# Optimization experiments

Measured on AMD Instinct MI355X. Metric: run time of the kernel, lower is better.

## Reference

```python
import jax, jax.numpy as jnp
import numpy as np

EMBED_DIM = 1024
NUM_HEADS = 16
RANK = 32
HEAD_DIM = EMBED_DIM // NUM_HEADS
SCALE = 1.0 / np.sqrt(RANK).astype(np.float32)


def setup_inputs() -> dict:
    key = jax.random.key(0)
    ks = jax.random.split(key, 9)
    B, S = 2, 2048
    def lin(k, fan_in, fan_out):
        bound = 1.0 / np.sqrt(fan_in)
        return jax.random.uniform(k, (fan_in, fan_out), jnp.float32, -bound, bound)
    return {
        "hidden_states": jax.random.normal(ks[0], (B, S, EMBED_DIM), jnp.float32),
        "Wq": lin(ks[1], EMBED_DIM, RANK * NUM_HEADS),
        "bq": jnp.zeros((RANK * NUM_HEADS,), jnp.float32),
        "Wk": lin(ks[2], EMBED_DIM, RANK * NUM_HEADS),
        "bk": jnp.zeros((RANK * NUM_HEADS,), jnp.float32),
        "Wv": lin(ks[3], EMBED_DIM, EMBED_DIM),
        "bv": jnp.zeros((EMBED_DIM,), jnp.float32),
        "Wo": lin(ks[4], EMBED_DIM, EMBED_DIM),
        "bo": jnp.zeros((EMBED_DIM,), jnp.float32),
    }


def reference(hidden_states, Wq, bq, Wk, bk, Wv, bv, Wo, bo):
    B, S, E = hidden_states.shape
    q = (hidden_states @ Wq + bq).reshape(B, S, NUM_HEADS, RANK)      # [b,i,h,r]
    k = (hidden_states @ Wk + bk).reshape(B, S, NUM_HEADS, RANK)      # [b,j,h,r]
    v = (hidden_states @ Wv + bv).reshape(B, S, NUM_HEADS, HEAD_DIM)  # [b,j,h,d]
    # full [b,i,j,h] score tensor, softmax over j (axis=2), as in the torch code
    scores = jnp.einsum('bihr,bjhr->bijh', q, k) * SCALE
    attn = jax.nn.softmax(scores, axis=2)
    out = jnp.einsum('bijh,bjhd->bihd', attn, v).reshape(B, S, E)
    return out @ Wo + bo
```

## Files before the change

### kernel.cpp

```cpp
#include <hip/hip_runtime.h>

#define EMBED   1024
#define NHEADS  16
#define RANK    32
#define HDIM    64
#define BATCH   2
#define SEQ     2048
#define BSQ     (BATCH * SEQ)
#define CEXP    0.25505998f

typedef __attribute__((ext_vector_type(8))) short bf16x8;
typedef __attribute__((ext_vector_type(4))) float f32x4;
typedef __attribute__((ext_vector_type(8))) _Float16 f16x8;

__device__ __forceinline__ float bf2f(unsigned short u) {
    union { unsigned int i; float f; } x; x.i = ((unsigned int)u) << 16;
    return x.f;
}
__device__ __forceinline__ unsigned short f2bf(float f) {
    union { float f; unsigned int i; } x; x.f = f;
    unsigned int r = x.i + 0x7FFFu + ((x.i >> 16) & 1u);
    return (unsigned short)(r >> 16);
}

#define ASYNC16(gp, lp) \
    __builtin_amdgcn_global_load_lds( \
        (const __attribute__((address_space(1))) void*)(gp), \
        (__attribute__((address_space(3))) void*)(lp), 16, 0, 0)

__global__ __launch_bounds__(256) void prep_all(
    const float* __restrict__ hs,
    const float* __restrict__ Wq, const float* __restrict__ Wk,
    const float* __restrict__ Wv, const float* __restrict__ Wo,
    const float* __restrict__ bq, const float* __restrict__ bk,
    const float* __restrict__ bv,
    unsigned short* __restrict__ hsb, unsigned short* __restrict__ wT_all,
    unsigned short* __restrict__ woT, float* __restrict__ ball)
{
    __shared__ float L[64][65];
    const int blk = blockIdx.x;
    const int t = threadIdx.x;

    if (blk < 2048) {
        const size_t i = ((size_t)blk * 256 + t) * 8;
        float4 v0 = *(const float4*)(hs + i);
        float4 v1 = *(const float4*)(hs + i + 4);
        ushort4 o0, o1;
        o0.x = f2bf(v0.x); o0.y = f2bf(v0.y); o0.z = f2bf(v0.z); o0.w = f2bf(v0.w);
        o1.x = f2bf(v1.x); o1.y = f2bf(v1.y); o1.z = f2bf(v1.z); o1.w = f2bf(v1.w);
        *(ushort4*)(hsb + i) = o0;
        *(ushort4*)(hsb + i + 4) = o1;
        return;
    }
    if (blk < 2816) {
        int idx = blk - 2048;
        int z, bx, by;
        if (idx < 256) { z = idx >> 7; int r2 = idx & 127; bx = r2 & 7; by = r2 >> 3; }
        else { idx -= 256; z = 2 + (idx >> 8); int r2 = idx & 255; bx = r2 & 15; by = r2 >> 4; }
        const int Nw = (z < 2) ? 512 : 1024;
        const float* W = (z == 0) ? Wq : (z == 1) ? Wk : (z == 2) ? Wv : Wo;
        unsigned short* dst = (z == 3) ? woT : (wT_all + (size_t)z * 512 * 1024);

        const int r = t >> 2, c0 = (t & 3) * 16;
        const float* src = W + (size_t)(by * 64 + r) * Nw + bx * 64 + c0;
        #pragma unroll
        for (int u = 0; u < 4; u++)
            *(float4*)&L[r][c0 + 4 * u] = *(const float4*)(src + 4 * u);
        __syncthreads();
        unsigned short* drow = dst + (size_t)(bx * 64 + r) * 1024 + by * 64 + c0;
        #pragma unroll
        for (int u4 = 0; u4 < 4; u4++) {
            ushort4 o;
            o.x = f2bf(L[c0 + 4 * u4 + 0][r]);
            o.y = f2bf(L[c0 + 4 * u4 + 1][r]);
            o.z = f2bf(L[c0 + 4 * u4 + 2][r]);
            o.w = f2bf(L[c0 + 4 * u4 + 3][r]);
            *(ushort4*)(drow + 4 * u4) = o;
        }
        return;
    }
    {
        const int i = (blk - 2816) * 256 + t;
        ball[i] = (i < 512) ? bq[i] : (i < 1024) ? bk[i - 512] : bv[i - 1024];
    }
}

template <bool OUT_F32>
__global__ __launch_bounds__(256) void gemm_mfma(
    const unsigned short* __restrict__ A, const unsigned short* __restrict__ BT,
    const float* __restrict__ bias, void* __restrict__ Cv,
    unsigned short* __restrict__ qH, unsigned short* __restrict__ kH,
    unsigned short* __restrict__ vTout, int N)
{
    __shared__ unsigned short As[128 * 32];
    __shared__ unsigned short Bs[128 * 32];
    const int K = 1024;
    const int t = threadIdx.x;
    const int lane = t & 63;
    const int li = lane & 15, la = lane >> 4;
    const int w = t >> 6, wm = w >> 1, wn = w & 1;
    const int row0 = blockIdx.y * 128, col0 = blockIdx.x * 128;

    const int sr = lane >> 2, sc2 = (lane & 3) * 8;
    const unsigned short* ag0 = A + (size_t)(row0 + w * 32 + sr) * K + sc2;
    const unsigned short* ag1 = A + (size_t)(row0 + w * 32 + 16 + sr) * K + sc2;
    const unsigned short* bg0 = BT + (size_t)(col0 + w * 32 + sr) * K + sc2;
    const unsigned short* bg1 = BT + (size_t)(col0 + w * 32 + 16 + sr) * K + sc2;
    unsigned short* lA0 = &As[(w * 32) * 32];
    unsigned short* lA1 = &As[(w * 32 + 16) * 32];
    unsigned short* lB0 = &Bs[(w * 32) * 32];
    unsigned short* lB1 = &Bs[(w * 32 + 16) * 32];

    f32x4 acc[4][4];
    #pragma unroll
    for (int i = 0; i < 4; i++)
        #pragma unroll
        for (int j = 0; j < 4; j++)
            acc[i][j] = (f32x4){0.f, 0.f, 0.f, 0.f};

    for (int k0 = 0; k0 < K; k0 += 32) {
        ASYNC16(ag0 + k0, lA0);
        ASYNC16(ag1 + k0, lA1);
        ASYNC16(bg0 + k0, lB0);
        ASYNC16(bg1 + k0, lB1);
        __syncthreads();
        bf16x8 af[4], bfr[4];
        #pragma unroll
        for (int mt = 0; mt < 4; mt++)
            af[mt] = *(const bf16x8*)&As[(wm * 64 + mt * 16 + li) * 32 + la * 8];
        #pragma unroll
        for (int nt = 0; nt < 4; nt++)
            bfr[nt] = *(const bf16x8*)&Bs[(wn * 64 + nt * 16 + li) * 32 + la * 8];
        #pragma unroll
        for (int mt = 0; mt < 4; mt++)
            #pragma unroll
            for (int nt = 0; nt < 4; nt++)
                acc[mt][nt] = __builtin_amdgcn_mfma_f32_16x16x32_bf16(af[mt], bfr[nt], acc[mt][nt], 0, 0, 0);
        __syncthreads();
    }

    if (OUT_F32) {
        #pragma unroll
        for (int nt = 0; nt < 4; nt++) {
            const int col = col0 + wn * 64 + nt * 16 + li;
            const float bval = bias[col];
            #pragma unroll
            for (int mt = 0; mt < 4; mt++)
                #pragma unroll
                for (int r = 0; r < 4; r++) {
                    const int row = row0 + wm * 64 + mt * 16 + la * 4 + r;
                    ((float*)Cv)[(size_t)row * N + col] = acc[mt][nt][r] + bval;
                }
        }
    } else {
        const int bb = row0 >> 11;
        const int jb = (row0 & 2047) + wm * 64;
        #pragma unroll
        for (int nt = 0; nt < 4; nt++) {
            const int col = col0 + wn * 64 + nt * 16 + li;
            const float bval = bias[col];
            if (col < 1024) {
                const int hh = (col & 511) >> 5;
                const int rr = col & 31;
                unsigned short* base = ((col < 512) ? qH : kH)
                    + ((size_t)(bb * 16 + hh) * 2048) * 32 + rr;
                #pragma unroll
                for (int mt = 0; mt < 4; mt++)
                    #pragma unroll
                    for (int r = 0; r < 4; r++)
                        base[(size_t)(jb + mt * 16 + la * 4 + r) * 32] =
                            f2bf(acc[mt][nt][r] + bval);
            } else {
                const int hd = col - 1024;
                unsigned short* dcol = vTout + ((size_t)(bb * 16 + (hd >> 6)) * 64 + (hd & 63)) * SEQ;
                #pragma unroll
                for (int mt = 0; mt < 4; mt++) {
                    const int srow = jb + mt * 16 + la * 4;
                    ushort4 o;
                    o.x = f2bf(acc[mt][nt][0] + bval);
                    o.y = f2bf(acc[mt][nt][1] + bval);
                    o.z = f2bf(acc[mt][nt][2] + bval);
                    o.w = f2bf(acc[mt][nt][3] + bval);
                    *(ushort4*)(dcol + srow) = o;
                }
            }
        }
    }
}

__global__ __launch_bounds__(256) void attn_mfma(
    const unsigned short* __restrict__ qH,
    const unsigned short* __restrict__ kH,
    const unsigned short* __restrict__ vT,
    _Float16* __restrict__ Opart, float* __restrict__ lpart)
{
    __shared__ unsigned short kt[64 * 32];
    __shared__ unsigned short vt[64 * 72];
    __shared__ unsigned short P[64 * 72];

    const int t = threadIdx.x;
    const int lane = t & 63;
    const int li = lane & 15, la = lane >> 4;
    const int w = t >> 6;

    const int blk = blockIdx.x;
    const int jh = blk & 1;
    const int itile = (blk >> 1) & 31;
    const int bh = blk >> 6;
    const int i0 = itile * 64;
    const int jbase = jh * 1024;

    bf16x8 qfrag;
    {
        const unsigned short* qp = qH + ((size_t)bh * 2048 + i0 + w * 16 + li) * 32 + la * 8;
        ushort4 q0 = *(const ushort4*)qp;
        ushort4 q1 = *(const ushort4*)(qp + 4);
        short u[8];
        u[0] = (short)f2bf(bf2f(q0.x) * CEXP);
        u[1] = (short)f2bf(bf2f(q0.y) * CEXP);
        u[2] = (short)f2bf(bf2f(q0.z) * CEXP);
        u[3] = (short)f2bf(bf2f(q0.w) * CEXP);
        u[4] = (short)f2bf(bf2f(q1.x) * CEXP);
        u[5] = (short)f2bf(bf2f(q1.y) * CEXP);
        u[6] = (short)f2bf(bf2f(q1.z) * CEXP);
        u[7] = (short)f2bf(bf2f(q1.w) * CEXP);
        qfrag = *(const bf16x8*)u;
    }

    const unsigned short* kbase = kH + (size_t)bh * 2048 * 32;
    const unsigned short* vbase = vT + (size_t)bh * 64 * SEQ;

    const int ks_off = t * 8;
    const int vs_row = t >> 3, vs_c = (t & 7) * 8;

    f32x4 accO[4];
    #pragma unroll
    for (int dt = 0; dt < 4; dt++) accO[dt] = (f32x4){0.f, 0.f, 0.f, 0.f};
    float l_part = 0.f;
    const int prow = w * 16 + li;

    uint4 kreg = *(const uint4*)(kbase + (size_t)jbase * 32 + ks_off);
    uint4 vreg0 = *(const uint4*)(vbase + (size_t)vs_row * SEQ + jbase + vs_c);
    uint4 vreg1 = *(const uint4*)(vbase + (size_t)(vs_row + 32) * SEQ + jbase + vs_c);

    for (int j0 = jbase; j0 < jbase + 1024; j0 += 64) {
        __syncthreads();
        *(uint4*)&kt[ks_off] = kreg;
        *(uint4*)&vt[vs_row * 72 + vs_c] = vreg0;
        *(uint4*)&vt[(vs_row + 32) * 72 + vs_c] = vreg1;
        __syncthreads();

        const int jn = (j0 + 64 < jbase + 1024) ? j0 + 64 : jbase;
        kreg = *(const uint4*)(kbase + (size_t)jn * 32 + ks_off);
        vreg0 = *(const uint4*)(vbase + (size_t)vs_row * SEQ + jn + vs_c);
        vreg1 = *(const uint4*)(vbase + (size_t)(vs_row + 32) * SEQ + jn + vs_c);

        f32x4 sc[4];
        #pragma unroll
        for (int jt = 0; jt < 4; jt++) {
            const bf16x8 kf = *(const bf16x8*)&kt[(jt * 16 + li) * 32 + la * 8];
            sc[jt] = __builtin_amdgcn_mfma_f32_16x16x32_bf16(kf, qfrag, (f32x4){0.f, 0.f, 0.f, 0.f}, 0, 0, 0);
        }

        #pragma unroll
        for (int jt = 0; jt < 4; jt++) {
            union { float f; unsigned int u; } c0, c1, c2, c3;
            c0.f = exp2f(sc[jt][0]);
            c1.f = exp2f(sc[jt][1]);
            c2.f = exp2f(sc[jt][2]);
            c3.f = exp2f(sc[jt][3]);
            l_part += (c0.f + c1.f) + (c2.f + c3.f);
            uint2 pk;
            pk.x = __builtin_amdgcn_perm(c1.u + 0x8000u, c0.u + 0x8000u, 0x07060302u);
            pk.y = __builtin_amdgcn_perm(c3.u + 0x8000u, c2.u + 0x8000u, 0x07060302u);
            *(uint2*)&P[prow * 72 + jt * 16 + la * 4] = pk;
        }

        #pragma unroll
        for (int ksl = 0; ksl < 2; ksl++) {
            const bf16x8 pf = *(const bf16x8*)&P[prow * 72 + ksl * 32 + la * 8];
            #pragma unroll
            for (int dt = 0; dt < 4; dt++) {
                const bf16x8 vf = *(const bf16x8*)&vt[(dt * 16 + li) * 72 + ksl * 32 + la * 8];
                accO[dt] = __builtin_amdgcn_mfma_f32_16x16x32_bf16(pf, vf, accO[dt], 0, 0, 0);
            }
        }
    }

    l_part += __shfl_xor(l_part, 16);
    l_part += __shfl_xor(l_part, 32);

    _Float16* ob = Opart + (size_t)blk * 4096;
    #pragma unroll
    for (int dt = 0; dt < 4; dt++)
        #pragma unroll
        for (int r = 0; r < 4; r++)
            ob[(w * 16 + la * 4 + r) * 64 + dt * 16 + li] = (_Float16)accO[dt][r];
    if (la == 0) lpart[(size_t)blk * 64 + w * 16 + li] = l_part;
}

__global__ __launch_bounds__(256) void attn_combine(
    const _Float16* __restrict__ Op, const float* __restrict__ lp,
    unsigned short* __restrict__ ao)
{
    const int c = blockIdx.x;
    const int t = threadIdx.x;
    const int bh = c >> 5, itile = c & 31;
    const int b = bh >> 4, h = bh & 15;
    const int i = t >> 2, d0 = (t & 3) * 16;

    const float linv = 1.f / (lp[(size_t)c * 128 + i] + lp[(size_t)c * 128 + 64 + i]);
    const _Float16* a0 = Op + (size_t)c * 8192 + i * 64 + d0;
    const _Float16* a1 = a0 + 4096;
    unsigned short* dst = ao + ((size_t)(b * SEQ + itile * 64 + i)) * 1024 + h * 64 + d0;

    #pragma unroll
    for (int u = 0; u < 2; u++) {
        f16x8 x0 = *(const f16x8*)(a0 + u * 8);
        f16x8 x1 = *(const f16x8*)(a1 + u * 8);
        ushort4 o0, o1;
        o0.x = f2bf(((float)x0[0] + (float)x1[0]) * linv);
        o0.y = f2bf(((float)x0[1] + (float)x1[1]) * linv);
        o0.z = f2bf(((float)x0[2] + (float)x1[2]) * linv);
        o0.w = f2bf(((float)x0[3] + (float)x1[3]) * linv);
        o1.x = f2bf(((float)x0[4] + (float)x1[4]) * linv);
        o1.y = f2bf(((float)x0[5] + (float)x1[5]) * linv);
        o1.z = f2bf(((float)x0[6] + (float)x1[6]) * linv);
        o1.w = f2bf(((float)x0[7] + (float)x1[7]) * linv);
        *(ushort4*)(dst + u * 8) = o0;
        *(ushort4*)(dst + u * 8 + 4) = o1;
    }
}

extern "C" void kernel_launch(void* const* d_in, const int* in_sizes, int n_in,
                              void* d_out, int out_size, void* d_ws, size_t ws_size,
                              hipStream_t stream) {
    const float* hs = (const float*)d_in[0];
    const float* Wq = (const float*)d_in[1];
    const float* bq = (const float*)d_in[2];
    const float* Wk = (const float*)d_in[3];
    const float* bk = (const float*)d_in[4];
    const float* Wv = (const float*)d_in[5];
    const float* bv = (const float*)d_in[6];
    const float* Wo = (const float*)d_in[7];
    const float* bo = (const float*)d_in[8];

    char* p = (char*)d_ws;
    _Float16*       Opart = (_Float16*)p;
    unsigned short* hsb   = (unsigned short*)p;
    unsigned short* wT    = (unsigned short*)(p + (8u << 20));
    float*          lpart = (float*)(p + (16u << 20));
    unsigned short* woT   = (unsigned short*)(p + 17834048u - 532544u + 0u);
    woT   = (unsigned short*)(p + 17301504u);
    float*          ball  = (float*)(p + 19398656u);
    unsigned short* qHb   = (unsigned short*)(p + 19406848u);
    unsigned short* kHb   = (unsigned short*)(p + 23601152u);
    unsigned short* vTb   = (unsigned short*)(p + 27795456u);
    unsigned short* ao    = (unsigned short*)(p + 36184064u);

    prep_all<<<dim3(2824), 256, 0, stream>>>(hs, Wq, Wk, Wv, Wo, bq, bk, bv,
                                             hsb, wT, woT, ball);

    gemm_mfma<false><<<dim3(16, 32), 256, 0, stream>>>(
        hsb, wT, ball, nullptr, qHb, kHb, vTb, 2048);

    attn_mfma<<<dim3(BATCH * NHEADS * 32 * 2), 256, 0, stream>>>(qHb, kHb, vTb, Opart, lpart);

    attn_combine<<<dim3(BATCH * NHEADS * 32), 256, 0, stream>>>(Opart, lpart, ao);

    gemm_mfma<true><<<dim3(8, 32), 256, 0, stream>>>(
        ao, woT, bo, d_out, nullptr, nullptr, nullptr, 1024);
}
```

Baseline: 203.8 us.

## Split key range across waves in attention, drop combine kernel, retile output GEMM

Rewrites attention so that each block handles 32 query rows and its four waves each take an interleaved slice of the keys. K and V fragments are loaded straight from global memory into registers rather than staged through LDS. The softmax denominator is computed with an MFMA against a ones vector, and the per-wave partial outputs are reduced in LDS before being normalized and written as bf16, which removes the separate combine kernel and its fp16 partial buffers. The output projection GEMM moves to 64-row tiles to launch more blocks. The risks are more uncoalesced global loads for K and V, and extra LDS round-trips and barriers in the reduction epilogue.

```diff
diff --git a/kernel.cpp b/kernel.cpp
--- a/kernel.cpp
+++ b/kernel.cpp
@@ -11,7 +11,6 @@
 
 typedef __attribute__((ext_vector_type(8))) short bf16x8;
 typedef __attribute__((ext_vector_type(4))) float f32x4;
-typedef __attribute__((ext_vector_type(8))) _Float16 f16x8;
 
 __device__ __forceinline__ float bf2f(unsigned short u) {
     union { unsigned int i; float f; } x; x.i = ((unsigned int)u) << 16;
@@ -85,12 +84,11 @@
     }
 }
 
-template <bool OUT_F32>
-__global__ __launch_bounds__(256) void gemm_mfma(
+__global__ __launch_bounds__(256) void gemm_qkv(
     const unsigned short* __restrict__ A, const unsigned short* __restrict__ BT,
-    const float* __restrict__ bias, void* __restrict__ Cv,
+    const float* __restrict__ bias,
     unsigned short* __restrict__ qH, unsigned short* __restrict__ kH,
-    unsigned short* __restrict__ vTout, int N)
+    unsigned short* __restrict__ vTout)
 {
     __shared__ unsigned short As[128 * 32];
     __shared__ unsigned short Bs[128 * 32];
@@ -139,80 +137,126 @@
         __syncthreads();
     }
 
-    if (OUT_F32) {
-        #pragma unroll
-        for (int nt = 0; nt < 4; nt++) {
-            const int col = col0 + wn * 64 + nt * 16 + li;
-            const float bval = bias[col];
+    const int bb = row0 >> 11;
+    const int jb = (row0 & 2047) + wm * 64;
+    #pragma unroll
+    for (int nt = 0; nt < 4; nt++) {
+        const int col = col0 + wn * 64 + nt * 16 + li;
+        const float bval = bias[col];
+        if (col < 1024) {
+            const int hh = (col & 511) >> 5;
+            const int rr = col & 31;
+            unsigned short* base = ((col < 512) ? qH : kH)
+                + ((size_t)(bb * 16 + hh) * 2048) * 32 + rr;
             #pragma unroll
             for (int mt = 0; mt < 4; mt++)
                 #pragma unroll
-                for (int r = 0; r < 4; r++) {
-                    const int row = row0 + wm * 64 + mt * 16 + la * 4 + r;
-                    ((float*)Cv)[(size_t)row * N + col] = acc[mt][nt][r] + bval;
-                }
-        }
-    } else {
-        const int bb = row0 >> 11;
-        const int jb = (row0 & 2047) + wm * 64;
-        #pragma unroll
-        for (int nt = 0; nt < 4; nt++) {
-            const int col = col0 + wn * 64 + nt * 16 + li;
-            const float bval = bias[col];
-            if (col < 1024) {
-                const int hh = (col & 511) >> 5;
-                const int rr = col & 31;
-                unsigned short* base = ((col < 512) ? qH : kH)
-                    + ((size_t)(bb * 16 + hh) * 2048) * 32 + rr;
-                #pragma unroll
-                for (int mt = 0; mt < 4; mt++)
-                    #pragma unroll
-                    for (int r = 0; r < 4; r++)
-                        base[(size_t)(jb + mt * 16 + la * 4 + r) * 32] =
-                            f2bf(acc[mt][nt][r] + bval);
-            } else {
-                const int hd = col - 1024;
-                unsigned short* dcol = vTout + ((size_t)(bb * 16 + (hd >> 6)) * 64 + (hd & 63)) * SEQ;
-                #pragma unroll
-                for (int mt = 0; mt < 4; mt++) {
-                    const int srow = jb + mt * 16 + la * 4;
-                    ushort4 o;
-                    o.x = f2bf(acc[mt][nt][0] + bval);
-                    o.y = f2bf(acc[mt][nt][1] + bval);
-                    o.z = f2bf(acc[mt][nt][2] + bval);
-                    o.w = f2bf(acc[mt][nt][3] + bval);
-                    *(ushort4*)(dcol + srow) = o;
-                }
+                for (int r = 0; r < 4; r++)
+                    base[(size_t)(jb + mt * 16 + la * 4 + r) * 32] =
+                        f2bf(acc[mt][nt][r] + bval);
+        } else {
+            const int hd = col - 1024;
+            unsigned short* dcol = vTout + ((size_t)(bb * 16 + (hd >> 6)) * 64 + (hd & 63)) * SEQ;
+            #pragma unroll
+            for (int mt = 0; mt < 4; mt++) {
+                const int srow = jb + mt * 16 + la * 4;
+                ushort4 o;
+                o.x = f2bf(acc[mt][nt][0] + bval);
+                o.y = f2bf(acc[mt][nt][1] + bval);
+                o.z = f2bf(acc[mt][nt][2] + bval);
+                o.w = f2bf(acc[mt][nt][3] + bval);
+                *(ushort4*)(dcol + srow) = o;
             }
         }
     }
 }
 
-__global__ __launch_bounds__(256) void attn_mfma(
+__global__ __launch_bounds__(256) void gemm_out(
+    const unsigned short* __restrict__ A, const unsigned short* __restrict__ BT,
+    const float* __restrict__ bias, float* __restrict__ C)
+{
+    __shared__ unsigned short As[64 * 32];
+    __shared__ unsigned short Bs[128 * 32];
+    const int K = 1024;
+    const int t = threadIdx.x;
+    const int lane = t & 63;
+    const int li = lane & 15, la = lane >> 4;
+    const int w = t >> 6, wm = w >> 1, wn = w & 1;
+    const int row0 = blockIdx.y * 64, col0 = blockIdx.x * 128;
+
+    const int sr = lane >> 2, sc2 = (lane & 3) * 8;
+    const unsigned short* ag0 = A + (size_t)(row0 + w * 16 + sr) * K + sc2;
+    const unsigned short* bg0 = BT + (size_t)(col0 + w * 32 + sr) * K + sc2;
+    const unsigned short* bg1 = BT + (size_t)(col0 + w * 32 + 16 + sr) * K + sc2;
+    unsigned short* lA0 = &As[(w * 16) * 32];
+    unsigned short* lB0 = &Bs[(w * 32) * 32];
+    unsigned short* lB1 = &Bs[(w * 32 + 16) * 32];
+
+    f32x4 acc[2][4];
+    #pragma unroll
+    for (int i = 0; i < 2; i++)
+        #pragma unroll
+        for (int j = 0; j < 4; j++)
+            acc[i][j] = (f32x4){0.f, 0.f, 0.f, 0.f};
+
+    for (int k0 = 0; k0 < K; k0 += 32) {
+        ASYNC16(ag0 + k0, lA0);
+        ASYNC16(bg0 + k0, lB0);
+        ASYNC16(bg1 + k0, lB1);
+        __syncthreads();
+        bf16x8 af[2], bfr[4];
+        #pragma unroll
+        for (int mt = 0; mt < 2; mt++)
+            af[mt] = *(const bf16x8*)&As[(wm * 32 + mt * 16 + li) * 32 + la * 8];
+        #pragma unroll
+        for (int nt = 0; nt < 4; nt++)
+            bfr[nt] = *(const bf16x8*)&Bs[(wn * 64 + nt * 16 + li) * 32 + la * 8];
+        #pragma unroll
+        for (int mt = 0; mt < 2; mt++)
+            #pragma unroll
+            for (int nt = 0; nt < 4; nt++)
+                acc[mt][nt] = __builtin_amdgcn_mfma_f32_16x16x32_bf16(af[mt], bfr[nt], acc[mt][nt], 0, 0, 0);
+        __syncthreads();
+    }
+
+    #pragma unroll
+    for (int nt = 0; nt < 4; nt++) {
+        const int col = col0 + wn * 64 + nt * 16 + li;
+        const float bval = bias[col];
+        #pragma unroll
+        for (int mt = 0; mt < 2; mt++)
+            #pragma unroll
+            for (int r = 0; r < 4; r++) {
+                const int row = row0 + wm * 32 + mt * 16 + la * 4 + r;
+                C[(size_t)row * 1024 + col] = acc[mt][nt][r] + bval;
+            }
+    }
+}
+
+__global__ __launch_bounds__(256, 3) void attn_v5(
     const unsigned short* __restrict__ qH,
     const unsigned short* __restrict__ kH,
     const unsigned short* __restrict__ vT,
-    _Float16* __restrict__ Opart, float* __restrict__ lpart)
+    unsigned short* __restrict__ ao)
 {
-    __shared__ unsigned short kt[64 * 32];
-    __shared__ unsigned short vt[64 * 72];
-    __shared__ unsigned short P[64 * 72];
+    __shared__ float smem[2688];
+    unsigned short* P = (unsigned short*)smem;
+    float* lbuf = smem + 2560;
 
     const int t = threadIdx.x;
     const int lane = t & 63;
     const int li = lane & 15, la = lane >> 4;
     const int w = t >> 6;
 
-    const int blk = blockIdx.x;
-    const int jh = blk & 1;
-    const int itile = (blk >> 1) & 31;
-    const int bh = blk >> 6;
-    const int i0 = itile * 64;
-    const int jbase = jh * 1024;
-
-    bf16x8 qfrag;
-    {
-        const unsigned short* qp = qH + ((size_t)bh * 2048 + i0 + w * 16 + li) * 32 + la * 8;
+    const int bh = blockIdx.x & 31;
+    const int itile = blockIdx.x >> 5;
+    const int i0 = itile * 32;
+    const int b = bh >> 4, h = bh & 15;
+
+    bf16x8 qf[2];
+    #pragma unroll
+    for (int it = 0; it < 2; it++) {
+        const unsigned short* qp = qH + ((size_t)bh * 2048 + i0 + it * 16 + li) * 32 + la * 8;
         ushort4 q0 = *(const ushort4*)qp;
         ushort4 q1 = *(const ushort4*)(qp + 4);
         short u[8];
@@ -224,111 +268,109 @@
         u[5] = (short)f2bf(bf2f(q1.y) * CEXP);
         u[6] = (short)f2bf(bf2f(q1.z) * CEXP);
         u[7] = (short)f2bf(bf2f(q1.w) * CEXP);
-        qfrag = *(const bf16x8*)u;
-    }
-
-    const unsigned short* kbase = kH + (size_t)bh * 2048 * 32;
-    const unsigned short* vbase = vT + (size_t)bh * 64 * SEQ;
-
-    const int ks_off = t * 8;
-    const int vs_row = t >> 3, vs_c = (t & 7) * 8;
-
-    f32x4 accO[4];
-    #pragma unroll
-    for (int dt = 0; dt < 4; dt++) accO[dt] = (f32x4){0.f, 0.f, 0.f, 0.f};
-    float l_part = 0.f;
-    const int prow = w * 16 + li;
-
-    uint4 kreg = *(const uint4*)(kbase + (size_t)jbase * 32 + ks_off);
-    uint4 vreg0 = *(const uint4*)(vbase + (size_t)vs_row * SEQ + jbase + vs_c);
-    uint4 vreg1 = *(const uint4*)(vbase + (size_t)(vs_row + 32) * SEQ + jbase + vs_c);
-
-    for (int j0 = jbase; j0 < jbase + 1024; j0 += 64) {
-        __syncthreads();
-        *(uint4*)&kt[ks_off] = kreg;
-        *(uint4*)&vt[vs_row * 72 + vs_c] = vreg0;
-        *(uint4*)&vt[(vs_row + 32) * 72 + vs_c] = vreg1;
-        __syncthreads();
-
-        const int jn = (j0 + 64 < jbase + 1024) ? j0 + 64 : jbase;
-        kreg = *(const uint4*)(kbase + (size_t)jn * 32 + ks_off);
-        vreg0 = *(const uint4*)(vbase + (size_t)vs_row * SEQ + jn + vs_c);
-        vreg1 = *(const uint4*)(vbase + (size_t)(vs_row + 32) * SEQ + jn + vs_c);
-
-        f32x4 sc[4];
-        #pragma unroll
-        for (int jt = 0; jt < 4; jt++) {
-            const bf16x8 kf = *(const bf16x8*)&kt[(jt * 16 + li) * 32 + la * 8];
-            sc[jt] = __builtin_amdgcn_mfma_f32_16x16x32_bf16(kf, qfrag, (f32x4){0.f, 0.f, 0.f, 0.f}, 0, 0, 0);
+        qf[it] = *(const bf16x8*)u;
+    }
+
+    bf16x8 vones;
+    #pragma unroll
+    for (int u2 = 0; u2 < 8; u2++) vones[u2] = (short)0x3F80;
+
+    const unsigned short* kbase = kH + (size_t)bh * 2048 * 32
+                                  + (size_t)(w * 32 + li) * 32 + la * 8;
+    const unsigned short* vbase = vT + (size_t)bh * 64 * SEQ
+                                  + (size_t)li * SEQ + w * 32 + la * 8;
+
+    unsigned short* Pw = P + w * 32 * 40;
+
+    f32x4 accO[2][4], accl[2];
+    #pragma unroll
+    for (int mt = 0; mt < 2; mt++) {
+        accl[mt] = (f32x4){0.f, 0.f, 0.f, 0.f};
+        #pragma unroll
+        for (int dt = 0; dt < 4; dt++) accO[mt][dt] = (f32x4){0.f, 0.f, 0.f, 0.f};
+    }
+
+    bf16x8 kf0 = *(const bf16x8*)(kbase);
+    bf16x8 kf1 = *(const bf16x8*)(kbase + 512);
+
+    for (int j0 = 0; j0 < SEQ; j0 += 128) {
+        bf16x8 vf[4];
+        #pragma unroll
+        for (int dt = 0; dt < 4; dt++)
+            vf[dt] = *(const bf16x8*)(vbase + (size_t)dt * 16 * SEQ + j0);
+        const int jn = (j0 + 128) & 2047;
+        const bf16x8 kn0 = *(const bf16x8*)(kbase + (size_t)jn * 32);
+        const bf16x8 kn1 = *(const bf16x8*)(kbase + (size_t)jn * 32 + 512);
+
+        f32x4 sc[2][2];
+        sc[0][0] = __builtin_amdgcn_mfma_f32_16x16x32_bf16(kf0, qf[0], (f32x4){0.f,0.f,0.f,0.f}, 0, 0, 0);
+        sc[0][1] = __builtin_amdgcn_mfma_f32_16x16x32_bf16(kf0, qf[1], (f32x4){0.f,0.f,0.f,0.f}, 0, 0, 0);
+        sc[1][0] = __builtin_amdgcn_mfma_f32_16x16x32_bf16(kf1, qf[0], (f32x4){0.f,0.f,0.f,0.f}, 0, 0, 0);
+        sc[1][1] = __builtin_amdgcn_mfma_f32_16x16x32_bf16(kf1, qf[1], (f32x4){0.f,0.f,0.f,0.f}, 0, 0, 0);
+
+        #pragma unroll
+        for (int jt = 0; jt < 2; jt++)
+            #pragma unroll
+            for (int it = 0; it < 2; it++) {
+                union { float f; unsigned int u; } c0, c1, c2, c3;
+                c0.f = exp2f(sc[jt][it][0]);
+                c1.f = exp2f(sc[jt][it][1]);
+                c2.f = exp2f(sc[jt][it][2]);
+                c3.f = exp2f(sc[jt][it][3]);
+                uint2 pk;
+                pk.x = __builtin_amdgcn_perm(c1.u + 0x8000u, c0.u + 0x8000u, 0x07060302u);
+                pk.y = __builtin_amdgcn_perm(c3.u + 0x8000u, c2.u + 0x8000u, 0x07060302u);
+                *(uint2*)&Pw[(it * 16 + li) * 40 + jt * 16 + la * 4] = pk;
+            }
+
+        #pragma unroll
+        for (int mt = 0; mt < 2; mt++) {
+            const bf16x8 af = *(const bf16x8*)&Pw[(mt * 16 + li) * 40 + la * 8];
+            accl[mt] = __builtin_amdgcn_mfma_f32_16x16x32_bf16(af, vones, accl[mt], 0, 0, 0);
+            #pragma unroll
+            for (int dt = 0; dt < 4; dt++)
+                accO[mt][dt] = __builtin_amdgcn_mfma_f32_16x16x32_bf16(af, vf[dt], accO[mt][dt], 0, 0, 0);
         }
-
-        #pragma unroll
-        for (int jt = 0; jt < 4; jt++) {
-            union { float f; unsigned int u; } c0, c1, c2, c3;
-            c0.f = exp2f(sc[jt][0]);
-            c1.f = exp2f(sc[jt][1]);
-            c2.f = exp2f(sc[jt][2]);
-            c3.f = exp2f(sc[jt][3]);
-            l_part += (c0.f + c1.f) + (c2.f + c3.f);
-            uint2 pk;
-            pk.x = __builtin_amdgcn_perm(c1.u + 0x8000u, c0.u + 0x8000u, 0x07060302u);
-            pk.y = __builtin_amdgcn_perm(c3.u + 0x8000u, c2.u + 0x8000u, 0x07060302u);
-            *(uint2*)&P[prow * 72 + jt * 16 + la * 4] = pk;
+        kf0 = kn0; kf1 = kn1;
+    }
+
+    if (li == 0) {
+        #pragma unroll
+        for (int mt = 0; mt < 2; mt++) {
+            float4 tv;
+            tv.x = accl[mt][0]; tv.y = accl[mt][1];
+            tv.z = accl[mt][2]; tv.w = accl[mt][3];
+            *(float4*)&lbuf[w * 32 + mt * 16 + la * 4] = tv;
         }
-
-        #pragma unroll
-        for (int ksl = 0; ksl < 2; ksl++) {
-            const bf16x8 pf = *(const bf16x8*)&P[prow * 72 + ksl * 32 + la * 8];
-            #pragma unroll
-            for (int dt = 0; dt < 4; dt++) {
-                const bf16x8 vf = *(const bf16x8*)&vt[(dt * 16 + li) * 72 + ksl * 32 + la * 8];
-                accO[dt] = __builtin_amdgcn_mfma_f32_16x16x32_bf16(pf, vf, accO[dt], 0, 0, 0);
-            }
+    }
+    __syncthreads();
+
+    const int ir = w * 8 + (lane >> 3);
+    const int dl = (lane & 7) * 2;
+    const float lsum = lbuf[ir] + lbuf[32 + ir] + lbuf[64 + ir] + lbuf[96 + ir];
+    const float linv = 1.0f / lsum;
+    float* obuf = smem;
+    unsigned short* aorow = ao + ((size_t)(b * SEQ + i0 + ir)) * 1024 + h * 64 + dl;
+
+    #pragma unroll
+    for (int s = 0; s < 4; s++) {
+        float* ow = obuf + w * 512;
+        #pragma unroll
+        for (int mt = 0; mt < 2; mt++)
+            #pragma unroll
+            for (int r = 0; r < 4; r++)
+                ow[(mt * 16 + la * 4 + r) * 16 + li] = accO[mt][s][r];
+        __syncthreads();
+        float v0 = 0.f, v1 = 0.f;
+        #pragma unroll
+        for (int w2 = 0; w2 < 4; w2++) {
+            const float2 x = *(const float2*)&obuf[w2 * 512 + ir * 16 + dl];
+            v0 += x.x; v1 += x.y;
         }
-    }
-
-    l_part += __shfl_xor(l_part, 16);
-    l_part += __shfl_xor(l_part, 32);
-
-    _Float16* ob = Opart + (size_t)blk * 4096;
-    #pragma unroll
-    for (int dt = 0; dt < 4; dt++)
-        #pragma unroll
-        for (int r = 0; r < 4; r++)
-            ob[(w * 16 + la * 4 + r) * 64 + dt * 16 + li] = (_Float16)accO[dt][r];
-    if (la == 0) lpart[(size_t)blk * 64 + w * 16 + li] = l_part;
-}
-
-__global__ __launch_bounds__(256) void attn_combine(
-    const _Float16* __restrict__ Op, const float* __restrict__ lp,
-    unsigned short* __restrict__ ao)
-{
-    const int c = blockIdx.x;
-    const int t = threadIdx.x;
-    const int bh = c >> 5, itile = c & 31;
-    const int b = bh >> 4, h = bh & 15;
-    const int i = t >> 2, d0 = (t & 3) * 16;
-
-    const float linv = 1.f / (lp[(size_t)c * 128 + i] + lp[(size_t)c * 128 + 64 + i]);
-    const _Float16* a0 = Op + (size_t)c * 8192 + i * 64 + d0;
-    const _Float16* a1 = a0 + 4096;
-    unsigned short* dst = ao + ((size_t)(b * SEQ + itile * 64 + i)) * 1024 + h * 64 + d0;
-
-    #pragma unroll
-    for (int u = 0; u < 2; u++) {
-        f16x8 x0 = *(const f16x8*)(a0 + u * 8);
-        f16x8 x1 = *(const f16x8*)(a1 + u * 8);
-        ushort4 o0, o1;
-        o0.x = f2bf(((float)x0[0] + (float)x1[0]) * linv);
-        o0.y = f2bf(((float)x0[1] + (float)x1[1]) * linv);
-        o0.z = f2bf(((float)x0[2] + (float)x1[2]) * linv);
-        o0.w = f2bf(((float)x0[3] + (float)x1[3]) * linv);
-        o1.x = f2bf(((float)x0[4] + (float)x1[4]) * linv);
-        o1.y = f2bf(((float)x0[5] + (float)x1[5]) * linv);
-        o1.z = f2bf(((float)x0[6] + (float)x1[6]) * linv);
-        o1.w = f2bf(((float)x0[7] + (float)x1[7]) * linv);
-        *(ushort4*)(dst + u * 8) = o0;
-        *(ushort4*)(dst + u * 8 + 4) = o1;
+        const unsigned int outp = (unsigned int)f2bf(v0 * linv)
+                                | ((unsigned int)f2bf(v1 * linv) << 16);
+        *(unsigned int*)(aorow + s * 16) = outp;
+        __syncthreads();
     }
 }
 
@@ -346,28 +388,21 @@
     const float* bo = (const float*)d_in[8];
 
     char* p = (char*)d_ws;
-    _Float16*       Opart = (_Float16*)p;
-    unsigned short* hsb   = (unsigned short*)p;
-    unsigned short* wT    = (unsigned short*)(p + (8u << 20));
-    float*          lpart = (float*)(p + (16u << 20));
-    unsigned short* woT   = (unsigned short*)(p + 17834048u - 532544u + 0u);
-    woT   = (unsigned short*)(p + 17301504u);
-    float*          ball  = (float*)(p + 19398656u);
-    unsigned short* qHb   = (unsigned short*)(p + 19406848u);
-    unsigned short* kHb   = (unsigned short*)(p + 23601152u);
-    unsigned short* vTb   = (unsigned short*)(p + 27795456u);
-    unsigned short* ao    = (unsigned short*)(p + 36184064u);
+    unsigned short* hsb = (unsigned short*)(p);
+    unsigned short* wT  = (unsigned short*)(p + 8388608u);
+    unsigned short* woT = (unsigned short*)(p + 12582912u);
+    float*          ball= (float*)(p + 14680064u);
+    unsigned short* qHb = (unsigned short*)(p + 14688256u);
+    unsigned short* kHb = (unsigned short*)(p + 18882560u);
+    unsigned short* vTb = (unsigned short*)(p + 23076864u);
+    unsigned short* ao  = (unsigned short*)(p + 31465472u);
 
     prep_all<<<dim3(2824), 256, 0, stream>>>(hs, Wq, Wk, Wv, Wo, bq, bk, bv,
                                              hsb, wT, woT, ball);
 
-    gemm_mfma<false><<<dim3(16, 32), 256, 0, stream>>>(
-        hsb, wT, ball, nullptr, qHb, kHb, vTb, 2048);
-
-    attn_mfma<<<dim3(BATCH * NHEADS * 32 * 2), 256, 0, stream>>>(qHb, kHb, vTb, Opart, lpart);
-
-    attn_combine<<<dim3(BATCH * NHEADS * 32), 256, 0, stream>>>(Opart, lpart, ao);
-
-    gemm_mfma<true><<<dim3(8, 32), 256, 0, stream>>>(
-        ao, woT, bo, d_out, nullptr, nullptr, nullptr, 1024);
-}
+    gemm_qkv<<<dim3(16, 32), 256, 0, stream>>>(hsb, wT, ball, qHb, kHb, vTb);
+
+    attn_v5<<<dim3(2048), 256, 0, stream>>>(qHb, kHb, vTb, ao);
+
+    gemm_out<<<dim3(8, 64), 256, 0, stream>>>(ao, woT, bo, (float*)d_out);
+}
```

Result: slower. 211.9 us (+4.0%).
